# Kernel optimization log

Hardware: AMD Instinct MI355X
Metric: run time of the kernel (lower is better)

The kernel has to match this reference:

```python
import jax, jax.numpy as jnp
import numpy as np

ALPHA = 0.2          # LeakyReLU negative slope
NEG_INF = -9e15      # mask value used by the original module


def setup_inputs() -> dict:
    key = jax.random.key(0)
    k1, k2, k3, k4 = jax.random.split(key, 4)
    N, Din, Dout = 8192, 512, 256
    features = jax.random.normal(k1, (N, Din), dtype=jnp.float32)
    adj = jax.random.randint(k2, (N, N), 0, 2, dtype=jnp.int32)
    W = jax.random.normal(k3, (Din, Dout), dtype=jnp.float32) * (1.414 / np.sqrt(Din))
    a = jax.random.normal(k4, (2 * Dout, 1), dtype=jnp.float32) * (1.414 / np.sqrt(2 * Dout))
    return {"features": features, "adj": adj, "W": W, "a": a}


def reference(features, adj, W, a):
    Dout = W.shape[1]
    Wh = features @ W                       # [N, Dout]
    # e_ij = leakyrelu([Wh_i || Wh_j] @ a) decomposes additively:
    # identical math to the N*N*2D concat in the original, without materializing it.
    src = Wh @ a[:Dout, 0]                  # [N]  contribution of node i
    dst = Wh @ a[Dout:, 0]                  # [N]  contribution of node j
    e = jax.nn.leaky_relu(src[:, None] + dst[None, :], negative_slope=ALPHA)  # [N, N]
    masked = jnp.where(adj > 0, e, NEG_INF)
    attention = jax.nn.softmax(masked, axis=1)   # dropout p=0.0 (eval) -> identity
    h_prime = attention @ Wh                # [N, Dout]
    return jax.nn.elu(h_prime)
```

## Files before the change

### kernel.cpp

```cpp
#include <hip/hip_runtime.h>
#include <hip/hip_bf16.h>

#define NN   8192
#define DIN  512
#define DOUT 256

typedef __attribute__((ext_vector_type(8))) short s16x8;
typedef __attribute__((ext_vector_type(4))) float f32x4;

static __device__ __forceinline__ unsigned short f2bf(float f) {
    union { float f; unsigned u; } v; v.f = f;
    unsigned r = v.u + 0x7fffu + ((v.u >> 16) & 1u);
    return (unsigned short)(r >> 16);
}

static __device__ __forceinline__ void gload_lds16(const void* g, void* l) {
    __builtin_amdgcn_global_load_lds(
        (const __attribute__((address_space(1))) unsigned int*)g,
        (__attribute__((address_space(3))) unsigned int*)l, 16, 0, 0);
}

__global__ __launch_bounds__(256) void k_wh2(const float* __restrict__ feat,
                                             const float* __restrict__ W,
                                             const float* __restrict__ a,
                                             unsigned short* __restrict__ WhT,
                                             float* __restrict__ src,
                                             float* __restrict__ dst) {
    __shared__ float lf[16 * DIN];
    __shared__ float red[2][4][16];
    const int tid = threadIdx.x;
    const int i0  = blockIdx.x * 16;
    const int w   = tid >> 6, lane = tid & 63;

    const float4* fsrc = (const float4*)(feat + (size_t)i0 * DIN);
    float4* fdst = (float4*)lf;
    #pragma unroll
    for (int q = 0; q < 8; ++q) fdst[tid + q * 256] = fsrc[tid + q * 256];
    __syncthreads();

    const int c = tid;
    float outs[16];
    #pragma unroll
    for (int r = 0; r < 16; ++r) outs[r] = 0.f;

    for (int k = 0; k < DIN; k += 4) {
        float w0 = W[(k + 0) * DOUT + c];
        float w1 = W[(k + 1) * DOUT + c];
        float w2 = W[(k + 2) * DOUT + c];
        float w3 = W[(k + 3) * DOUT + c];
        #pragma unroll
        for (int r = 0; r < 16; ++r) {
            float4 f = *(const float4*)&lf[r * DIN + k];
            outs[r] = fmaf(f.x, w0, fmaf(f.y, w1, fmaf(f.z, w2, fmaf(f.w, w3, outs[r]))));
        }
    }

    unsigned short tb[16];
    #pragma unroll
    for (int r = 0; r < 16; ++r) tb[r] = f2bf(outs[r]);
    uint4* wt = (uint4*)(WhT + (size_t)c * NN + i0);
    wt[0] = *(uint4*)&tb[0];
    wt[1] = *(uint4*)&tb[8];

    const float as_ = a[c], ad_ = a[DOUT + c];
    #pragma unroll
    for (int r = 0; r < 16; ++r) {
        float s = outs[r] * as_;
        float d = outs[r] * ad_;
        #pragma unroll
        for (int off = 32; off; off >>= 1) {
            s += __shfl_xor(s, off);
            d += __shfl_xor(d, off);
        }
        if (lane == 0) { red[0][w][r] = s; red[1][w][r] = d; }
    }
    __syncthreads();
    if (tid < 16)
        src[i0 + tid] = red[0][0][tid] + red[0][1][tid] + red[0][2][tid] + red[0][3][tid];
    else if (tid < 32) {
        int r = tid - 16;
        dst[i0 + r] = red[1][0][r] + red[1][1][r] + red[1][2][r] + red[1][3][r];
    }
}


#define ATTN_STEP(RD, WR, CUR, NXT, T)                                                   \
{                                                                                        \
    const int k0_ = (T) * 64;                                                            \
    if ((T) < 31) {                                                                      \
        const int kn_ = k0_ + 64;                                                        \
        NXT[0][0][0] = *(const int4*)(adjR0 + kn_);                                      \
        NXT[0][0][1] = *(const int4*)(adjR0 + kn_ + 4);                                  \
        NXT[0][1][0] = *(const int4*)(adjR0 + kn_ + 32);                                 \
        NXT[0][1][1] = *(const int4*)(adjR0 + kn_ + 36);                                 \
        NXT[1][0][0] = *(const int4*)(adjR1 + kn_);                                      \
        NXT[1][0][1] = *(const int4*)(adjR1 + kn_ + 4);                                  \
        NXT[1][1][0] = *(const int4*)(adjR1 + kn_ + 32);                                 \
        NXT[1][1][1] = *(const int4*)(adjR1 + kn_ + 36);                                 \
        const size_t gkb_ = (size_t)(kb0 + kn_) * 2;                                     \
        _Pragma("unroll")                                                                \
        for (int q = 0; q < 4; ++q)                                                      \
            gload_lds16((const char*)WhT + (size_t)rowB[q] * (NN * 2) + gkb_ + kbB[q],   \
                        (char*)(WR) + (q * 512 + tid) * 16);                             \
    }                                                                                    \
    _Pragma("unroll")                                                                    \
    for (int h = 0; h < 2; ++h) {                                                        \
        const int kh_ = k0_ + h * 32 + koff;                                             \
        float4 d0_ = *(const float4*)&ldsD[kh_];                                         \
        float4 d1_ = *(const float4*)&ldsD[kh_ + 4];                                     \
        float dd_[8] = {d0_.x, d0_.y, d0_.z, d0_.w, d1_.x, d1_.y, d1_.z, d1_.w};         \
        s16x8 afm[2];                                                                    \
        _Pragma("unroll")                                                                \
        for (int m = 0; m < 2; ++m) {                                                    \
            int avv[8] = {CUR[m][h][0].x, CUR[m][h][0].y, CUR[m][h][0].z, CUR[m][h][0].w,\
                          CUR[m][h][1].x, CUR[m][h][1].y, CUR[m][h][1].z, CUR[m][h][1].w};\
            float pd_ = 0.f;                                                             \
            _Pragma("unroll")                                                            \
            for (int jj = 0; jj < 8; ++jj) {                                             \
                float x_ = si[m] + dd_[jj];                                              \
                x_ = fmaxf(x_, 0.2f * x_);                                               \
                float p_ = avv[jj] > 0 ? __expf(x_) : 0.f;                               \
                pd_ += p_;                                                               \
                afm[m][jj] = (short)f2bf(p_);                                            \
            }                                                                            \
            den[m] += pd_;                                                               \
        }                                                                                \
        const int kwh_ = h * 64 + lk * 16;                                               \
        _Pragma("unroll")                                                                \
        for (int n = 0; n < 8; ++n) {                                                    \
            const int col_ = c0 + n * 16 + cl;                                           \
            s16x8 bfv = *(const s16x8*)((const char*)(RD) + col_ * 128 +                 \
                                        (kwh_ ^ ((col_ & 7) << 4)));                     \
            acc[0][n] = __builtin_amdgcn_mfma_f32_16x16x32_bf16(afm[0], bfv, acc[0][n], 0, 0, 0); \
            acc[1][n] = __builtin_amdgcn_mfma_f32_16x16x32_bf16(afm[1], bfv, acc[1][n], 0, 0, 0); \
        }                                                                                \
    }                                                                                    \
    __syncthreads();                                                                     \
}

__global__ __launch_bounds__(512, 2) void k_attn2(const int* __restrict__ adj,
                                                  const unsigned short* __restrict__ WhT,
                                                  const float* __restrict__ src,
                                                  const float* __restrict__ dstg,
                                                  float* __restrict__ denp,
                                                  float* __restrict__ part) {
    __shared__ __attribute__((aligned(16))) char Bs[2][32768];
    __shared__ float4 ldsD4[512];
    const float* ldsD = (const float*)ldsD4;

    const int tid = threadIdx.x;
    const int w   = tid >> 6, lane = tid & 63;
    const int cl  = lane & 15, lk = lane >> 4;
    const int koff = lk * 8;
    const int rg  = w >> 1, cg = w & 1;
    const int c0  = cg * 128;
    const int rt  = blockIdx.x & 63;
    const int ks  = blockIdx.x >> 6;
    const int kb0 = ks * 2048;
    const int rowbase = rt * 128 + rg * 32;
    const int ia0 = rowbase + cl;
    const int ia1 = rowbase + 16 + cl;

    const int* adjR0 = adj + (size_t)ia0 * NN + kb0 + koff;
    const int* adjR1 = adj + (size_t)ia1 * NN + kb0 + koff;

    float si[2];
    si[0] = src[ia0];
    si[1] = src[ia1];

    int rowB[4], kbB[4];
    #pragma unroll
    for (int q = 0; q < 4; ++q) {
        int chunk = q * 512 + tid;
        rowB[q] = chunk >> 3;
        kbB[q]  = ((chunk & 7) * 16) ^ ((rowB[q] & 7) << 4);
    }

    f32x4 acc[2][8];
    #pragma unroll
    for (int m = 0; m < 2; ++m)
        #pragma unroll
        for (int n = 0; n < 8; ++n) { acc[m][n][0]=0.f; acc[m][n][1]=0.f; acc[m][n][2]=0.f; acc[m][n][3]=0.f; }
    float den[2] = {0.f, 0.f};

    ldsD4[tid] = *(const float4*)(dstg + kb0 + tid * 4);
    #pragma unroll
    for (int q = 0; q < 4; ++q)
        gload_lds16((const char*)WhT + (size_t)rowB[q] * (NN * 2) + (size_t)kb0 * 2 + kbB[q],
                    (char*)Bs[0] + (q * 512 + tid) * 16);
    int4 Ca[2][2][2], Cb[2][2][2];
    Ca[0][0][0] = *(const int4*)(adjR0);      Ca[0][0][1] = *(const int4*)(adjR0 + 4);
    Ca[0][1][0] = *(const int4*)(adjR0 + 32); Ca[0][1][1] = *(const int4*)(adjR0 + 36);
    Ca[1][0][0] = *(const int4*)(adjR1);      Ca[1][0][1] = *(const int4*)(adjR1 + 4);
    Ca[1][1][0] = *(const int4*)(adjR1 + 32); Ca[1][1][1] = *(const int4*)(adjR1 + 36);
    __syncthreads();

    char* bufA = (char*)Bs[0];
    char* bufB = (char*)Bs[1];
    for (int it = 0; it < 16; ++it) {
        ATTN_STEP(bufA, bufB, Ca, Cb, 2 * it);
        ATTN_STEP(bufB, bufA, Cb, Ca, 2 * it + 1);
    }

    den[0] += __shfl_xor(den[0], 16); den[0] += __shfl_xor(den[0], 32);
    den[1] += __shfl_xor(den[1], 16); den[1] += __shfl_xor(den[1], 32);
    if (cg == 0 && lk == 0) {
        denp[(size_t)ks * NN + ia0] = den[0];
        denp[(size_t)ks * NN + ia1] = den[1];
    }

    float* pp = part + (size_t)ks * (NN * DOUT);
    #pragma unroll
    for (int m = 0; m < 2; ++m) {
        #pragma unroll
        for (int n = 0; n < 8; ++n) {
            const int colg = c0 + n * 16 + cl;
            #pragma unroll
            for (int q = 0; q < 4; ++q) {
                const int rowg = rowbase + m * 16 + lk * 4 + q;
                pp[(size_t)rowg * DOUT + colg] = acc[m][n][q];
            }
        }
    }
}

__global__ __launch_bounds__(256) void k_finish2(const float* __restrict__ part,
                                                 const float* __restrict__ denp,
                                                 float* __restrict__ out) {
    const int idx = blockIdx.x * 256 + threadIdx.x;
    const int row = idx >> 6;
    float den = denp[row] + denp[NN + row] + denp[2 * NN + row] + denp[3 * NN + row];
    float rv = den > 0.f ? 1.f / den : 0.f;
    const int st = NN * DOUT / 4;
    const float4* p = (const float4*)part;
    float4 va = p[idx], vb = p[idx + st], vc = p[idx + 2 * st], vd = p[idx + 3 * st];
    float4 s;
    s.x = (va.x + vb.x + vc.x + vd.x) * rv;
    s.y = (va.y + vb.y + vc.y + vd.y) * rv;
    s.z = (va.z + vb.z + vc.z + vd.z) * rv;
    s.w = (va.w + vb.w + vc.w + vd.w) * rv;
    s.x = s.x > 0.f ? s.x : expm1f(s.x);
    s.y = s.y > 0.f ? s.y : expm1f(s.y);
    s.z = s.z > 0.f ? s.z : expm1f(s.z);
    s.w = s.w > 0.f ? s.w : expm1f(s.w);
    ((float4*)out)[idx] = s;
}

extern "C" void kernel_launch(void* const* d_in, const int* in_sizes, int n_in,
                              void* d_out, int out_size, void* d_ws, size_t ws_size,
                              hipStream_t stream) {
    const float* feat = (const float*)d_in[0];
    const int*   adj  = (const int*)d_in[1];
    const float* W    = (const float*)d_in[2];
    const float* a    = (const float*)d_in[3];
    float* out = (float*)d_out;

    char* ws = (char*)d_ws;
    unsigned short* WhT  = (unsigned short*)ws;
    float*          src  = (float*)(ws + 4194304);
    float*          dst  = (float*)(ws + 4227072);
    float*          denp = (float*)(ws + 4259840);
    float*          part = (float*)(ws + 4390912);

    k_wh2    <<<512,  256, 0, stream>>>(feat, W, a, WhT, src, dst);
    k_attn2  <<<256,  512, 0, stream>>>(adj, WhT, src, dst, denp, part);
    k_finish2<<<2048, 256, 0, stream>>>(part, denp, out);
}
```

Baseline: 197.1 us.

## Restructure attention kernel: shared P tile in LDS with 32x32 MFMA

```diff
diff --git a/kernel.cpp b/kernel.cpp
--- a/kernel.cpp
+++ b/kernel.cpp
@@ -5,8 +5,8 @@
 #define DIN  512
 #define DOUT 256
 
-typedef __attribute__((ext_vector_type(8))) short s16x8;
-typedef __attribute__((ext_vector_type(4))) float f32x4;
+typedef __attribute__((ext_vector_type(8)))  short s16x8;
+typedef __attribute__((ext_vector_type(16))) float f32x16;
 
 static __device__ __forceinline__ unsigned short f2bf(float f) {
     union { float f; unsigned u; } v; v.f = f;
@@ -83,143 +83,111 @@
     }
 }
 
-
-#define ATTN_STEP(RD, WR, CUR, NXT, T)                                                   \
-{                                                                                        \
-    const int k0_ = (T) * 64;                                                            \
-    if ((T) < 31) {                                                                      \
-        const int kn_ = k0_ + 64;                                                        \
-        NXT[0][0][0] = *(const int4*)(adjR0 + kn_);                                      \
-        NXT[0][0][1] = *(const int4*)(adjR0 + kn_ + 4);                                  \
-        NXT[0][1][0] = *(const int4*)(adjR0 + kn_ + 32);                                 \
-        NXT[0][1][1] = *(const int4*)(adjR0 + kn_ + 36);                                 \
-        NXT[1][0][0] = *(const int4*)(adjR1 + kn_);                                      \
-        NXT[1][0][1] = *(const int4*)(adjR1 + kn_ + 4);                                  \
-        NXT[1][1][0] = *(const int4*)(adjR1 + kn_ + 32);                                 \
-        NXT[1][1][1] = *(const int4*)(adjR1 + kn_ + 36);                                 \
-        const size_t gkb_ = (size_t)(kb0 + kn_) * 2;                                     \
-        _Pragma("unroll")                                                                \
-        for (int q = 0; q < 4; ++q)                                                      \
-            gload_lds16((const char*)WhT + (size_t)rowB[q] * (NN * 2) + gkb_ + kbB[q],   \
-                        (char*)(WR) + (q * 512 + tid) * 16);                             \
-    }                                                                                    \
-    _Pragma("unroll")                                                                    \
-    for (int h = 0; h < 2; ++h) {                                                        \
-        const int kh_ = k0_ + h * 32 + koff;                                             \
-        float4 d0_ = *(const float4*)&ldsD[kh_];                                         \
-        float4 d1_ = *(const float4*)&ldsD[kh_ + 4];                                     \
-        float dd_[8] = {d0_.x, d0_.y, d0_.z, d0_.w, d1_.x, d1_.y, d1_.z, d1_.w};         \
-        s16x8 afm[2];                                                                    \
-        _Pragma("unroll")                                                                \
-        for (int m = 0; m < 2; ++m) {                                                    \
-            int avv[8] = {CUR[m][h][0].x, CUR[m][h][0].y, CUR[m][h][0].z, CUR[m][h][0].w,\
-                          CUR[m][h][1].x, CUR[m][h][1].y, CUR[m][h][1].z, CUR[m][h][1].w};\
-            float pd_ = 0.f;                                                             \
-            _Pragma("unroll")                                                            \
-            for (int jj = 0; jj < 8; ++jj) {                                             \
-                float x_ = si[m] + dd_[jj];                                              \
-                x_ = fmaxf(x_, 0.2f * x_);                                               \
-                float p_ = avv[jj] > 0 ? __expf(x_) : 0.f;                               \
-                pd_ += p_;                                                               \
-                afm[m][jj] = (short)f2bf(p_);                                            \
-            }                                                                            \
-            den[m] += pd_;                                                               \
-        }                                                                                \
-        const int kwh_ = h * 64 + lk * 16;                                               \
-        _Pragma("unroll")                                                                \
-        for (int n = 0; n < 8; ++n) {                                                    \
-            const int col_ = c0 + n * 16 + cl;                                           \
-            s16x8 bfv = *(const s16x8*)((const char*)(RD) + col_ * 128 +                 \
-                                        (kwh_ ^ ((col_ & 7) << 4)));                     \
-            acc[0][n] = __builtin_amdgcn_mfma_f32_16x16x32_bf16(afm[0], bfv, acc[0][n], 0, 0, 0); \
-            acc[1][n] = __builtin_amdgcn_mfma_f32_16x16x32_bf16(afm[1], bfv, acc[1][n], 0, 0, 0); \
-        }                                                                                \
-    }                                                                                    \
-    __syncthreads();                                                                     \
-}
-
-__global__ __launch_bounds__(512, 2) void k_attn2(const int* __restrict__ adj,
+__global__ __launch_bounds__(512, 4) void k_attn3(const int* __restrict__ adj,
                                                   const unsigned short* __restrict__ WhT,
                                                   const float* __restrict__ src,
                                                   const float* __restrict__ dstg,
                                                   float* __restrict__ denp,
                                                   float* __restrict__ part) {
     __shared__ __attribute__((aligned(16))) char Bs[2][32768];
-    __shared__ float4 ldsD4[512];
-    const float* ldsD = (const float*)ldsD4;
-
-    const int tid = threadIdx.x;
-    const int w   = tid >> 6, lane = tid & 63;
-    const int cl  = lane & 15, lk = lane >> 4;
-    const int koff = lk * 8;
-    const int rg  = w >> 1, cg = w & 1;
-    const int c0  = cg * 128;
-    const int rt  = blockIdx.x & 63;
-    const int ks  = blockIdx.x >> 6;
+    __shared__ __attribute__((aligned(16))) char Pl[8192];
+
+    const int tid  = threadIdx.x;
+    const int lane = tid & 63;
+    const int w    = tid >> 6;
+    const int l31  = lane & 31, lhi = lane >> 5;
+    const int c0w  = w * 32;
+
+    const int rt  = blockIdx.x & 127;
+    const int ks  = blockIdx.x >> 7;
     const int kb0 = ks * 2048;
-    const int rowbase = rt * 128 + rg * 32;
-    const int ia0 = rowbase + cl;
-    const int ia1 = rowbase + 16 + cl;
-
-    const int* adjR0 = adj + (size_t)ia0 * NN + kb0 + koff;
-    const int* adjR1 = adj + (size_t)ia1 * NN + kb0 + koff;
-
-    float si[2];
-    si[0] = src[ia0];
-    si[1] = src[ia1];
-
-    int rowB[4], kbB[4];
+
+    const int r  = tid >> 3, kb = tid & 7;
+    const int gr = rt * 64 + r;
+    const float si = src[gr];
+    const int*   adjR = adj  + (size_t)gr * NN + kb0 + kb * 8;
+    const float* dstp = dstg +                   kb0 + kb * 8;
+    const int pbyte = r * 128 + ((kb * 16) ^ ((r & 7) << 4));
+
+    int colB[4], kbB[4];
     #pragma unroll
     for (int q = 0; q < 4; ++q) {
         int chunk = q * 512 + tid;
-        rowB[q] = chunk >> 3;
-        kbB[q]  = ((chunk & 7) * 16) ^ ((rowB[q] & 7) << 4);
-    }
-
-    f32x4 acc[2][8];
-    #pragma unroll
-    for (int m = 0; m < 2; ++m)
-        #pragma unroll
-        for (int n = 0; n < 8; ++n) { acc[m][n][0]=0.f; acc[m][n][1]=0.f; acc[m][n][2]=0.f; acc[m][n][3]=0.f; }
-    float den[2] = {0.f, 0.f};
-
-    ldsD4[tid] = *(const float4*)(dstg + kb0 + tid * 4);
+        colB[q] = chunk >> 3;
+        kbB[q]  = ((chunk & 7) * 16) ^ ((colB[q] & 7) << 4);
+    }
+
+    f32x16 acc[2];
+    #pragma unroll
+    for (int mt = 0; mt < 2; ++mt)
+        #pragma unroll
+        for (int e = 0; e < 16; ++e) acc[mt][e] = 0.f;
+    float den = 0.f;
+
     #pragma unroll
     for (int q = 0; q < 4; ++q)
-        gload_lds16((const char*)WhT + (size_t)rowB[q] * (NN * 2) + (size_t)kb0 * 2 + kbB[q],
+        gload_lds16((const char*)WhT + (size_t)colB[q] * (NN * 2) + (size_t)kb0 * 2 + kbB[q],
                     (char*)Bs[0] + (q * 512 + tid) * 16);
-    int4 Ca[2][2][2], Cb[2][2][2];
-    Ca[0][0][0] = *(const int4*)(adjR0);      Ca[0][0][1] = *(const int4*)(adjR0 + 4);
-    Ca[0][1][0] = *(const int4*)(adjR0 + 32); Ca[0][1][1] = *(const int4*)(adjR0 + 36);
-    Ca[1][0][0] = *(const int4*)(adjR1);      Ca[1][0][1] = *(const int4*)(adjR1 + 4);
-    Ca[1][1][0] = *(const int4*)(adjR1 + 32); Ca[1][1][1] = *(const int4*)(adjR1 + 36);
+    int4 a0 = *(const int4*)(adjR);
+    int4 a1 = *(const int4*)(adjR + 4);
     __syncthreads();
 
-    char* bufA = (char*)Bs[0];
-    char* bufB = (char*)Bs[1];
-    for (int it = 0; it < 16; ++it) {
-        ATTN_STEP(bufA, bufB, Ca, Cb, 2 * it);
-        ATTN_STEP(bufB, bufA, Cb, Ca, 2 * it + 1);
-    }
-
-    den[0] += __shfl_xor(den[0], 16); den[0] += __shfl_xor(den[0], 32);
-    den[1] += __shfl_xor(den[1], 16); den[1] += __shfl_xor(den[1], 32);
-    if (cg == 0 && lk == 0) {
-        denp[(size_t)ks * NN + ia0] = den[0];
-        denp[(size_t)ks * NN + ia1] = den[1];
-    }
+    for (int t = 0; t < 32; ++t) {
+        const int cur = t & 1;
+        int4 na0, na1;
+        if (t < 31) {
+            na0 = *(const int4*)(adjR + (t + 1) * 64);
+            na1 = *(const int4*)(adjR + (t + 1) * 64 + 4);
+            const size_t gkb = (size_t)(kb0 + (t + 1) * 64) * 2;
+            #pragma unroll
+            for (int q = 0; q < 4; ++q)
+                gload_lds16((const char*)WhT + (size_t)colB[q] * (NN * 2) + gkb + kbB[q],
+                            (char*)Bs[cur ^ 1] + (q * 512 + tid) * 16);
+        }
+        float4 d0 = *(const float4*)(dstp + t * 64);
+        float4 d1 = *(const float4*)(dstp + t * 64 + 4);
+        const float dd[8] = {d0.x, d0.y, d0.z, d0.w, d1.x, d1.y, d1.z, d1.w};
+        const int   va[8] = {a0.x, a0.y, a0.z, a0.w, a1.x, a1.y, a1.z, a1.w};
+        s16x8 pw;
+        #pragma unroll
+        for (int jj = 0; jj < 8; ++jj) {
+            float x = si + dd[jj];
+            x = fmaxf(x, 0.2f * x);
+            float p = va[jj] > 0 ? __expf(x) : 0.f;
+            den += p;
+            pw[jj] = (short)f2bf(p);
+        }
+        *(s16x8*)(Pl + pbyte) = pw;
+        a0 = na0; a1 = na1;
+        __syncthreads();
+
+        #pragma unroll
+        for (int ks4 = 0; ks4 < 4; ++ks4) {
+            const int kbyte = ks4 * 32 + lhi * 16;
+            const int colg  = c0w + l31;
+            s16x8 bf = *(const s16x8*)(Bs[cur] + colg * 128 + (kbyte ^ ((colg & 7) << 4)));
+            #pragma unroll
+            for (int mt = 0; mt < 2; ++mt) {
+                const int row = mt * 32 + l31;
+                s16x8 af = *(const s16x8*)(Pl + row * 128 + (kbyte ^ ((row & 7) << 4)));
+                acc[mt] = __builtin_amdgcn_mfma_f32_32x32x16_bf16(af, bf, acc[mt], 0, 0, 0);
+            }
+        }
+        __syncthreads();
+    }
+
+    den += __shfl_xor(den, 1);
+    den += __shfl_xor(den, 2);
+    den += __shfl_xor(den, 4);
+    if ((tid & 7) == 0) denp[(size_t)ks * NN + gr] = den;
 
     float* pp = part + (size_t)ks * (NN * DOUT);
     #pragma unroll
-    for (int m = 0; m < 2; ++m) {
-        #pragma unroll
-        for (int n = 0; n < 8; ++n) {
-            const int colg = c0 + n * 16 + cl;
-            #pragma unroll
-            for (int q = 0; q < 4; ++q) {
-                const int rowg = rowbase + m * 16 + lk * 4 + q;
-                pp[(size_t)rowg * DOUT + colg] = acc[m][n][q];
-            }
+    for (int mt = 0; mt < 2; ++mt) {
+        #pragma unroll
+        for (int e = 0; e < 16; ++e) {
+            const int row = rt * 64 + mt * 32 + (e & 3) + 8 * (e >> 2) + 4 * lhi;
+            pp[(size_t)row * DOUT + c0w + l31] = acc[mt][e];
         }
     }
 }
@@ -263,6 +231,6 @@
     float*          part = (float*)(ws + 4390912);
 
     k_wh2    <<<512,  256, 0, stream>>>(feat, W, a, WhT, src, dst);
-    k_attn2  <<<256,  512, 0, stream>>>(adj, WhT, src, dst, denp, part);
+    k_attn3  <<<512,  512, 0, stream>>>(adj, WhT, src, dst, denp, part);
     k_finish2<<<2048, 256, 0, stream>>>(part, denp, out);
 }
```

After: 185.9 us. 5.7% less time.
